# Kernel optimization log

Measured on AMD Instinct MI355X. Metric: run time of the kernel, lower is better.

The kernel has to match this reference:

```python
import jax, jax.numpy as jnp
import numpy as np

T = 4096
EMBED = 1024
HEADS = 16


def setup_inputs() -> dict:
    key = jax.random.key(0)
    kx, kq, kk, kv = jax.random.split(key, 4)
    bound = 1.0 / np.sqrt(EMBED)
    x = jax.random.normal(kx, (T, EMBED), dtype=jnp.float32)
    Wq = jax.random.uniform(kq, (EMBED, EMBED), minval=-bound, maxval=bound, dtype=jnp.float32)
    Wk = jax.random.uniform(kk, (EMBED, EMBED), minval=-bound, maxval=bound, dtype=jnp.float32)
    Wv = jax.random.uniform(kv, (EMBED, EMBED), minval=-bound, maxval=bound, dtype=jnp.float32)
    return {"x": x, "Wq": Wq, "Wk": Wk, "Wv": Wv}


def reference(x, Wq, Wk, Wv):
    t, e = x.shape
    h = HEADS
    c = e // h  # head dim
    q = (x @ Wq).reshape(t, h, c)
    k = (x @ Wk).reshape(t, h, c)
    v = (x @ Wv).reshape(t, h, c)
    # scores: [h, t, t]
    scores = jnp.einsum('qhc,khc->hqk', q, k) / jnp.sqrt(jnp.asarray(c, x.dtype))
    causal = jnp.tril(jnp.ones((t, t), dtype=bool))
    scores = jnp.where(causal[None, :, :], scores, -jnp.inf)  # same as + log(tril)
    p = jax.nn.softmax(scores, axis=-1)
    y = jnp.einsum('hqk,khc->qhc', p, v)  # [t, h, c]
    return y.reshape(t, e)
```

## Files before the change

### kernel.cpp

```cpp
#include <hip/hip_runtime.h>
#include <hip/hip_bf16.h>

#define T_SEQ 4096
#define EMB 1024
#define NH 16
#define HD 64
#define QBLK 128
#define KVB 64
#define DEFER_THR 10.0f

typedef float f32x4 __attribute__((ext_vector_type(4)));
typedef float f32x16 __attribute__((ext_vector_type(16)));
typedef short short8 __attribute__((ext_vector_type(8)));
typedef short short4v __attribute__((ext_vector_type(4)));

__device__ inline unsigned short f2bf(float f) {
  union { float f; unsigned u; } a; a.f = f;
  unsigned r = a.u + 0x7fffu + ((a.u >> 16) & 1u);
  return (unsigned short)(r >> 16);
}
#if __has_builtin(__builtin_amdgcn_exp2f)
#define EXP2F(x) __builtin_amdgcn_exp2f(x)
#else
#define EXP2F(x) exp2f(x)
#endif
#define GLL16(g, l) __builtin_amdgcn_global_load_lds( \
    (const __attribute__((address_space(1))) void*)(g), \
    (__attribute__((address_space(3))) void*)(l), 16, 0, 0)

__global__ __launch_bounds__(256) void cast_x_kernel(const float* __restrict__ in,
                                                     unsigned short* __restrict__ out) {
  int i = (blockIdx.x * 256 + threadIdx.x) * 8;
  float4 a = *(const float4*)(in + i);
  float4 b = *(const float4*)(in + i + 4);
  uint4 o;
  o.x = f2bf(a.x) | ((unsigned)f2bf(a.y) << 16);
  o.y = f2bf(a.z) | ((unsigned)f2bf(a.w) << 16);
  o.z = f2bf(b.x) | ((unsigned)f2bf(b.y) << 16);
  o.w = f2bf(b.z) | ((unsigned)f2bf(b.w) << 16);
  *(uint4*)(out + i) = o;
}

__global__ __launch_bounds__(256) void transpose_cast_kernel(const float* __restrict__ Wq,
                                                             const float* __restrict__ Wk,
                                                             const float* __restrict__ Wv,
                                                             unsigned short* __restrict__ WTall) {
  int z = blockIdx.z;
  const float* W = (z == 0) ? Wq : ((z == 1) ? Wk : Wv);
  unsigned short* WT = WTall + (size_t)z * EMB * EMB;
  __shared__ unsigned short tile[32][33];
  int tx = threadIdx.x & 31, ty = threadIdx.x >> 5;
  int bn = blockIdx.x * 32, bk = blockIdx.y * 32;
#pragma unroll
  for (int p = 0; p < 4; p++)
    tile[ty + p * 8][tx] = f2bf(W[(size_t)(bk + ty + p * 8) * EMB + bn + tx]);
  __syncthreads();
#pragma unroll
  for (int p = 0; p < 4; p++)
    WT[(size_t)(bn + ty + p * 8) * EMB + bk + tx] = tile[tx][ty + p * 8];
}

__global__ __launch_bounds__(256) void gemm_qkv(const unsigned short* __restrict__ Xb,
                                                const unsigned short* __restrict__ WTall,
                                                unsigned short* __restrict__ QKV) {
  int z = blockIdx.z;
  const unsigned short* Bt = WTall + (size_t)z * EMB * EMB;
  unsigned short* Out = QKV + (size_t)z * T_SEQ * EMB;

  __shared__ __align__(16) unsigned short sA[128 * 32];
  __shared__ __align__(16) unsigned short sB[128 * 32];

  int m0 = blockIdx.x * 128, n0 = blockIdx.y * 128;
  int tid = threadIdx.x;
  int lane = tid & 63, wid = tid >> 6;
  int wr = wid >> 1, wc = wid & 1;
  int fr = lane & 15, fq = lane >> 4;

  int r0 = tid >> 2, o0 = (tid & 3) * 8;
  int r1 = (tid + 256) >> 2;

  f32x4 acc[4][4] = {};

  for (int k0 = 0; k0 < EMB; k0 += 32) {
    __syncthreads();
    GLL16(Xb + (size_t)(m0 + r0) * EMB + k0 + o0, sA + (size_t)tid * 8);
    GLL16(Xb + (size_t)(m0 + r1) * EMB + k0 + o0, sA + (size_t)(tid + 256) * 8);
    GLL16(Bt + (size_t)(n0 + r0) * EMB + k0 + o0, sB + (size_t)tid * 8);
    GLL16(Bt + (size_t)(n0 + r1) * EMB + k0 + o0, sB + (size_t)(tid + 256) * 8);
    asm volatile("s_waitcnt vmcnt(0)" ::: "memory");
    __syncthreads();

    short8 aF[4], bF[4];
#pragma unroll
    for (int i = 0; i < 4; i++) {
      aF[i] = *(const short8*)(sA + (wr * 64 + i * 16 + fr) * 32 + fq * 8);
      bF[i] = *(const short8*)(sB + (wc * 64 + i * 16 + fr) * 32 + fq * 8);
    }
#pragma unroll
    for (int i = 0; i < 4; i++)
#pragma unroll
      for (int j = 0; j < 4; j++)
        acc[i][j] = __builtin_amdgcn_mfma_f32_16x16x32_bf16(aF[i], bF[j], acc[i][j], 0, 0, 0);
  }

  if (z == 2) {
#pragma unroll
    for (int i = 0; i < 4; i++)
#pragma unroll
      for (int j = 0; j < 4; j++) {
        int col = n0 + wc * 64 + j * 16 + fr;
        int row0 = m0 + wr * 64 + i * 16 + fq * 4;
        short4v pk4;
#pragma unroll
        for (int r = 0; r < 4; r++) pk4[r] = (short)f2bf(acc[i][j][r]);
        *(short4v*)(Out + (size_t)col * T_SEQ + row0) = pk4;
      }
  } else {
    float scale = (z == 0) ? 0.1803368801111204f : 1.0f;
#pragma unroll
    for (int i = 0; i < 4; i++)
#pragma unroll
      for (int j = 0; j < 4; j++)
#pragma unroll
        for (int r = 0; r < 4; r++) {
          int row = m0 + wr * 64 + i * 16 + fq * 4 + r;
          int col = n0 + wc * 64 + j * 16 + fr;
          Out[(size_t)row * EMB + col] = f2bf(acc[i][j][r] * scale);
        }
  }
}

__global__ __launch_bounds__(256) void attn_kernel(const unsigned short* __restrict__ Qb,
                                                   const unsigned short* __restrict__ Kb,
                                                   const unsigned short* __restrict__ VTg,
                                                   float* __restrict__ out) {
  int qb = (gridDim.x - 1) - blockIdx.x;
  int h = blockIdx.y;
  int q0 = qb * QBLK;
  int tid = threadIdx.x;
  int lane = tid & 63, w = tid >> 6;
  int ql = lane & 31, hi = lane >> 5;

  __shared__ __align__(16) unsigned short smem[14336];
  unsigned short* sK = smem;
  unsigned short* sVT = smem + 64 * 72;
  unsigned short* sP = smem + 2 * 64 * 72 + w * (32 * 40);

  int wq0 = q0 + w * 32;
  int qg = wq0 + ql;

  short8 qf[4];
#pragma unroll
  for (int ks = 0; ks < 4; ks++)
    qf[ks] = *(const short8*)(Qb + (size_t)qg * EMB + h * HD + ks * 16 + hi * 8);

  f32x16 oT0 = {}, oT1 = {};
  float m = -1e30f, lsum = 0.f;

  int sr = tid >> 3;
  int scs = (tid & 7) * 8;

  int wqmax = wq0 + 31;
  int ntiles = (q0 + QBLK) / KVB;

  for (int t = 0; t < ntiles; t++) {
    int kv0 = t * KVB;
    short8 ka = *(const short8*)(Kb + (size_t)(kv0 + sr) * EMB + h * HD + scs);
    short8 kb = *(const short8*)(Kb + (size_t)(kv0 + sr + 32) * EMB + h * HD + scs);
    short8 va = *(const short8*)(VTg + (size_t)(h * HD + sr) * T_SEQ + kv0 + scs);
    short8 vb = *(const short8*)(VTg + (size_t)(h * HD + sr + 32) * T_SEQ + kv0 + scs);
    __syncthreads();
    *(short8*)(sK + sr * 72 + scs) = ka;
    *(short8*)(sK + (sr + 32) * 72 + scs) = kb;
    *(short8*)(sVT + sr * 72 + scs) = va;
    *(short8*)(sVT + (sr + 32) * 72 + scs) = vb;
    __syncthreads();

#pragma unroll
    for (int s = 0; s < 2; s++) {
      int kvs = kv0 + s * 32;
      if (kvs <= wqmax) {
        f32x16 st = {};
        __builtin_amdgcn_s_setprio(1);
#pragma unroll
        for (int ks = 0; ks < 4; ks++) {
          short8 kf = *(const short8*)(sK + (s * 32 + ql) * 72 + ks * 16 + hi * 8);
          st = __builtin_amdgcn_mfma_f32_32x32x16_bf16(kf, qf[ks], st, 0, 0, 0);
        }
        __builtin_amdgcn_s_setprio(0);
        if (kvs + 31 > wq0) {
#pragma unroll
          for (int r = 0; r < 16; r++) {
            int kvg = kvs + (r & 3) + 8 * (r >> 2) + 4 * hi;
            if (kvg > qg) st[r] = -1e30f;
          }
        }
        float mt = st[0];
#pragma unroll
        for (int r = 1; r < 16; r++) mt = fmaxf(mt, st[r]);
        mt = fmaxf(mt, __shfl_xor(mt, 32));
        if (!__all(mt - m <= DEFER_THR)) {
          float mnew = fmaxf(m, mt);
          float al = EXP2F(m - mnew);
          lsum *= al;
#pragma unroll
          for (int r = 0; r < 16; r++) { oT0[r] *= al; oT1[r] *= al; }
          m = mnew;
        }
#pragma unroll
        for (int r = 0; r < 16; r++) st[r] = EXP2F(st[r] - m);
        float ls = st[0];
#pragma unroll
        for (int r = 1; r < 16; r++) ls += st[r];
        ls += __shfl_xor(ls, 32);
        lsum += ls;

#pragma unroll
        for (int g = 0; g < 4; g++) {
          short4v pk4;
#pragma unroll
          for (int r4 = 0; r4 < 4; r4++) pk4[r4] = (short)f2bf(st[g * 4 + r4]);
          *(short4v*)(sP + ql * 40 + g * 8 + hi * 4) = pk4;
        }
        asm volatile("s_waitcnt lgkmcnt(0)" ::: "memory");
        __builtin_amdgcn_sched_barrier(0);

        __builtin_amdgcn_s_setprio(1);
#pragma unroll
        for (int ksp = 0; ksp < 2; ksp++) {
          short8 pa = *(const short8*)(sP + ql * 40 + ksp * 16 + hi * 8);
          int cb = s * 32 + ksp * 16 + hi * 8;
          short8 v0 = *(const short8*)(sVT + (0 * 32 + ql) * 72 + cb);
          short8 v1 = *(const short8*)(sVT + (1 * 32 + ql) * 72 + cb);
          oT0 = __builtin_amdgcn_mfma_f32_32x32x16_bf16(v0, pa, oT0, 0, 0, 0);
          oT1 = __builtin_amdgcn_mfma_f32_32x32x16_bf16(v1, pa, oT1, 0, 0, 0);
        }
        __builtin_amdgcn_s_setprio(0);
      }
    }
  }

  float inv = 1.0f / lsum;
  float* sw = (float*)smem + w * (32 * 36);
  int orow = lane >> 1, ocol = (lane & 1) * 16;
#pragma unroll
  for (int dt = 0; dt < 2; dt++) {
    __syncthreads();
#pragma unroll
    for (int r = 0; r < 16; r++) {
      int dl = (r & 3) + 8 * (r >> 2) + 4 * hi;
      sw[ql * 36 + dl] = (dt ? oT1[r] : oT0[r]) * inv;
    }
    __syncthreads();
#pragma unroll
    for (int c = 0; c < 4; c++) {
      f32x4 vv = *(const f32x4*)(sw + orow * 36 + ocol + c * 4);
      *(f32x4*)(out + (size_t)(wq0 + orow) * EMB + h * HD + dt * 32 + ocol + c * 4) = vv;
    }
  }
}

extern "C" void kernel_launch(void* const* d_in, const int* in_sizes, int n_in,
                              void* d_out, int out_size, void* d_ws, size_t ws_size,
                              hipStream_t stream) {
  const float* x  = (const float*)d_in[0];
  const float* Wq = (const float*)d_in[1];
  const float* Wk = (const float*)d_in[2];
  const float* Wv = (const float*)d_in[3];
  float* out = (float*)d_out;

  unsigned short* Qb = (unsigned short*)d_ws;
  unsigned short* Kb = Qb + (size_t)T_SEQ * EMB;
  unsigned short* VT = Kb + (size_t)T_SEQ * EMB;
  unsigned short* Xb = VT + (size_t)T_SEQ * EMB;
  unsigned short* WT = Xb + (size_t)T_SEQ * EMB;

  cast_x_kernel<<<(T_SEQ * EMB) / (256 * 8), 256, 0, stream>>>(x, Xb);
  dim3 tg(EMB / 32, EMB / 32, 3);
  transpose_cast_kernel<<<tg, 256, 0, stream>>>(Wq, Wk, Wv, WT);
  dim3 gg(T_SEQ / 128, EMB / 128, 3);
  gemm_qkv<<<gg, 256, 0, stream>>>(Xb, WT, Qb);
  dim3 ag(T_SEQ / QBLK, NH);
  attn_kernel<<<ag, 256, 0, stream>>>(Qb, Kb, VT, out);
}
```

Measured before the change: 258.6 us.

## Prefetch next K/V tile into registers and tree-reduce softmax max/sum

Loads the next KV tile's K and V^T fragments from global memory into registers right after the current tile is stored to LDS, so global latency overlaps the current tile's MFMA and softmax work. It also rewrites the per-row max and sum reductions as shallow trees to shorten dependency chains. It replaces manual float-to-bf16 rounding with packed bf16x2 conversion intrinsics. The prefetch keeps extra registers live across the compute loop, which may raise register pressure and lower occupancy.

```diff
diff --git a/kernel.cpp b/kernel.cpp
--- a/kernel.cpp
+++ b/kernel.cpp
@@ -163,18 +163,27 @@
   int wqmax = wq0 + 31;
   int ntiles = (q0 + QBLK) / KVB;
 
+  short8 ka = *(const short8*)(Kb + (size_t)(sr) * EMB + h * HD + scs);
+  short8 kb = *(const short8*)(Kb + (size_t)(sr + 32) * EMB + h * HD + scs);
+  short8 va = *(const short8*)(VTg + (size_t)(h * HD + sr) * T_SEQ + scs);
+  short8 vb = *(const short8*)(VTg + (size_t)(h * HD + sr + 32) * T_SEQ + scs);
+
   for (int t = 0; t < ntiles; t++) {
     int kv0 = t * KVB;
-    short8 ka = *(const short8*)(Kb + (size_t)(kv0 + sr) * EMB + h * HD + scs);
-    short8 kb = *(const short8*)(Kb + (size_t)(kv0 + sr + 32) * EMB + h * HD + scs);
-    short8 va = *(const short8*)(VTg + (size_t)(h * HD + sr) * T_SEQ + kv0 + scs);
-    short8 vb = *(const short8*)(VTg + (size_t)(h * HD + sr + 32) * T_SEQ + kv0 + scs);
     __syncthreads();
     *(short8*)(sK + sr * 72 + scs) = ka;
     *(short8*)(sK + (sr + 32) * 72 + scs) = kb;
     *(short8*)(sVT + sr * 72 + scs) = va;
     *(short8*)(sVT + (sr + 32) * 72 + scs) = vb;
     __syncthreads();
+
+    if (t + 1 < ntiles) {
+      int kv1 = kv0 + KVB;
+      ka = *(const short8*)(Kb + (size_t)(kv1 + sr) * EMB + h * HD + scs);
+      kb = *(const short8*)(Kb + (size_t)(kv1 + sr + 32) * EMB + h * HD + scs);
+      va = *(const short8*)(VTg + (size_t)(h * HD + sr) * T_SEQ + kv1 + scs);
+      vb = *(const short8*)(VTg + (size_t)(h * HD + sr + 32) * T_SEQ + kv1 + scs);
+    }
 
 #pragma unroll
     for (int s = 0; s < 2; s++) {
@@ -195,9 +204,12 @@
             if (kvg > qg) st[r] = -1e30f;
           }
         }
-        float mt = st[0];
-#pragma unroll
-        for (int r = 1; r < 16; r++) mt = fmaxf(mt, st[r]);
+        float a0 = fmaxf(fmaxf(st[0], st[1]), st[2]);
+        float a1 = fmaxf(fmaxf(st[3], st[4]), st[5]);
+        float a2 = fmaxf(fmaxf(st[6], st[7]), st[8]);
+        float a3 = fmaxf(fmaxf(st[9], st[10]), st[11]);
+        float a4 = fmaxf(fmaxf(st[12], st[13]), st[14]);
+        float mt = fmaxf(fmaxf(fmaxf(a0, a1), a2), fmaxf(fmaxf(a3, a4), st[15]));
         mt = fmaxf(mt, __shfl_xor(mt, 32));
         if (!__all(mt - m <= DEFER_THR)) {
           float mnew = fmaxf(m, mt);
@@ -209,18 +221,21 @@
         }
 #pragma unroll
         for (int r = 0; r < 16; r++) st[r] = EXP2F(st[r] - m);
-        float ls = st[0];
-#pragma unroll
-        for (int r = 1; r < 16; r++) ls += st[r];
+        float s0 = (st[0] + st[1]) + (st[2] + st[3]);
+        float s1 = (st[4] + st[5]) + (st[6] + st[7]);
+        float s2 = (st[8] + st[9]) + (st[10] + st[11]);
+        float s3 = (st[12] + st[13]) + (st[14] + st[15]);
+        float ls = (s0 + s1) + (s2 + s3);
         ls += __shfl_xor(ls, 32);
         lsum += ls;
 
 #pragma unroll
         for (int g = 0; g < 4; g++) {
-          short4v pk4;
-#pragma unroll
-          for (int r4 = 0; r4 < 4; r4++) pk4[r4] = (short)f2bf(st[g * 4 + r4]);
-          *(short4v*)(sP + ql * 40 + g * 8 + hi * 4) = pk4;
+          __hip_bfloat162 plo = __float22bfloat162_rn(float2{st[g * 4 + 0], st[g * 4 + 1]});
+          __hip_bfloat162 phi = __float22bfloat162_rn(float2{st[g * 4 + 2], st[g * 4 + 3]});
+          union { __hip_bfloat162 h[2]; short4v s4; } u4;
+          u4.h[0] = plo; u4.h[1] = phi;
+          *(short4v*)(sP + ql * 40 + g * 8 + hi * 4) = u4.s4;
         }
         asm volatile("s_waitcnt lgkmcnt(0)" ::: "memory");
         __builtin_amdgcn_sched_barrier(0);
```

Measured after the change: 251.0 us. 2.9% less time.
